# Performance work log

Hardware: AMD Instinct MI355X
Metric: run time of the kernel (lower is better)

Reference implementation:

```python
import jax, jax.numpy as jnp
import numpy as np

N = 100000   # nodes
E = 640000   # edges
F = 128      # num_features
H = 128      # hidden_channels
EPS = 1e-5   # BatchNorm1d eps
SCALE = 0.05


def setup_inputs() -> dict:
    key = jax.random.key(0)
    ks = jax.random.split(key, 16)
    inp = {
        "x": jax.random.normal(ks[0], (N, F), dtype=jnp.float32),
        "edge_index": jax.random.randint(ks[1], (2, E), 0, N, dtype=jnp.int32),
    }
    dims = [(F, H), (H, H), (H, H)]
    k = 2
    for i, (din, dout) in enumerate(dims):
        inp[f"Wl{i}"] = jax.random.normal(ks[k], (dout, din), dtype=jnp.float32) * SCALE
        inp[f"bl{i}"] = jax.random.normal(ks[k + 1], (dout,), dtype=jnp.float32) * SCALE
        inp[f"Wr{i}"] = jax.random.normal(ks[k + 2], (dout, din), dtype=jnp.float32) * SCALE
        k += 3
    inp["W1"] = jax.random.normal(ks[k], (H, H), dtype=jnp.float32) * SCALE
    inp["b1"] = jax.random.normal(ks[k + 1], (H,), dtype=jnp.float32) * SCALE
    inp["W2"] = jax.random.normal(ks[k + 2], (2, H), dtype=jnp.float32) * SCALE
    inp["b2"] = jax.random.normal(ks[k + 3], (2,), dtype=jnp.float32) * SCALE
    return inp


def _batchnorm(x):
    # BatchNorm1d(track_running_stats=False, affine=False): biased batch stats
    mu = jnp.mean(x, axis=0)
    var = jnp.var(x, axis=0)
    return (x - mu) / jnp.sqrt(var + EPS)


def _sage_conv(x, src, dst, Wl, bl, Wr):
    # PyG SAGEConv (aggr='mean'): out = lin_l(mean_agg(x[src] -> dst)) + lin_r(x)
    msg = x[src]                                             # [E, din]
    ssum = jax.ops.segment_sum(msg, dst, num_segments=N)     # [N, din]
    cnt = jax.ops.segment_sum(jnp.ones((E,), x.dtype), dst, num_segments=N)
    agg = ssum / jnp.maximum(cnt, 1.0)[:, None]              # mean, 0 for isolated
    return agg @ Wl.T + bl + x @ Wr.T


def reference(x, edge_index, Wl0, bl0, Wr0, Wl1, bl1, Wr1, Wl2, bl2, Wr2, W1, b1, W2, b2):
    src, dst = edge_index[0], edge_index[1]
    for Wl, bl, Wr in ((Wl0, bl0, Wr0), (Wl1, bl1, Wr1), (Wl2, bl2, Wr2)):
        x = jax.nn.relu(_batchnorm(_sage_conv(x, src, dst, Wl, bl, Wr)))
    x = jax.nn.relu(_batchnorm(x @ W1.T + b1))
    return x @ W2.T + b2
```

## Files before the change

kernel.cpp:

```cpp
#include <hip/hip_runtime.h>
#include <stdint.h>

typedef __bf16 v8bf __attribute__((ext_vector_type(8)));
typedef float f32x4 __attribute__((ext_vector_type(4)));
typedef float f32x2 __attribute__((ext_vector_type(2)));

__device__ __forceinline__ float b2f(unsigned short u) {
    unsigned int x = ((unsigned int)u) << 16;
    return __builtin_bit_cast(float, x);
}
__device__ __forceinline__ float b2f_lo(unsigned int v) {
    return __builtin_bit_cast(float, v << 16);
}
__device__ __forceinline__ float b2f_hi(unsigned int v) {
    return __builtin_bit_cast(float, v & 0xffff0000u);
}
__device__ __forceinline__ unsigned short f2b(float f) {
    unsigned int x = __builtin_bit_cast(unsigned int, f);
    unsigned int r = (x + 0x7fffu + ((x >> 16) & 1u)) >> 16;
    return (unsigned short)r;
}

__device__ __forceinline__ void load_lds16(const void* g, void* l) {
    __builtin_amdgcn_global_load_lds(
        (__attribute__((address_space(1))) void*)(const void*)g,
        (__attribute__((address_space(3))) void*)l, 16, 0, 0);
}

__device__ __forceinline__ void barrier_raw() {
    __builtin_amdgcn_sched_barrier(0);
    __builtin_amdgcn_s_barrier();
    __builtin_amdgcn_sched_barrier(0);
}

#define VMW(n) asm volatile("s_waitcnt vmcnt(" #n ")" ::: "memory")

struct WSrc { const float* p[7]; const float* s[6]; };

__global__ void k_prologue(WSrc w, unsigned short* __restrict__ wbuf,
                           const int* __restrict__ src, const int* __restrict__ dst,
                           int* __restrict__ pos, int* __restrict__ csr, int E,
                           const float* __restrict__ x, unsigned short* __restrict__ xcat,
                           unsigned short* __restrict__ y,
                           int n, int nFill, int nCvtw, int nCopyx) {
    int bid = blockIdx.x;
    int t = threadIdx.x;
    if (bid < nFill) {
        int i = bid * 256 + t;
        if (i < E) {
            int d = dst[i];
            int p = atomicAdd(&pos[d], 1);
            if (p < 64) csr[((size_t)d << 6) + p] = src[i];
        }
    } else if (bid < nFill + nCvtw) {
        int idx = (bid - nFill) * 256 + t;
        if (idx < 115458) {
            float v;
            if (idx < 114688) {
                v = w.p[idx >> 14][idx & 16383];
            } else {
                int rem = idx - 114688;
                int tt, j;
                if (rem < 512)      { tt = rem >> 7; j = rem & 127; }
                else if (rem < 768) { tt = 4; j = rem - 512; }
                else                { tt = 5; j = rem - 768; }
                v = w.s[tt][j];
            }
            wbuf[idx] = f2b(v);
        } else if (idx < 115458 + 64) {
            int k = idx - 115458;
            if (k < 32) {
                ushort4 z; z.x = z.y = z.z = z.w = 0;
                *(ushort4*)&xcat[(size_t)n * 256 + 128 + k * 4] = z;
            } else {
                ushort4 m; m.x = m.y = m.z = m.w = 0xFF7Fu;
                *(ushort4*)&y[(size_t)n * 128 + (k - 32) * 4] = m;
            }
        }
    } else {
        int T = nCopyx * 256;
        int tid = (bid - nFill - nCvtw) * 256 + t;
        int total = n * 32;
        for (int i0 = tid; i0 < total; i0 += 4 * T) {
#pragma unroll
            for (int u = 0; u < 4; u++) {
                int i = i0 + u * T;
                if (i < total) {
                    int row = i >> 5, c4 = (i & 31) * 4;
                    float4 v = *(const float4*)&x[(size_t)row * 128 + c4];
                    ushort4 o;
                    o.x = f2b(v.x); o.y = f2b(v.y); o.z = f2b(v.z); o.w = f2b(v.w);
                    *(ushort4*)&xcat[(size_t)row * 256 + 128 + c4] = o;
                }
            }
        }
    }
}

__global__ void k_hist(const int* __restrict__ pos, int* __restrict__ hist, int n) {
    __shared__ int lh[32];
    int t = threadIdx.x;
    int i = blockIdx.x * 256 + t;
    if (t < 32) lh[t] = 0;
    __syncthreads();
    if (i < n) atomicAdd(&lh[31 - min(pos[i], 31)], 1);
    __syncthreads();
    if (t < 32) atomicAdd(&hist[t], lh[t]);
}

__global__ void k_order(const int* __restrict__ cnt, const int* __restrict__ hist,
                        int* __restrict__ binpos, int* __restrict__ order, int n) {
    __shared__ int lh[32], gb[32], hloc[32];
    int t = threadIdx.x;
    if (t < 32) { lh[t] = 0; hloc[t] = hist[t]; }
    __syncthreads();
    int i = blockIdx.x * 256 + t;
    int b = 0, r = 0;
    if (i < n) {
        b = 31 - min(cnt[i], 31);
        r = atomicAdd(&lh[b], 1);
    }
    __syncthreads();
    if (t < 32) {
        int off = 0;
        for (int k = 0; k < t; k++) off += hloc[k];
        gb[t] = off + atomicAdd(&binpos[t], lh[t]);
    }
    __syncthreads();
    if (i < n) order[gb[b] + r] = i;
}

__global__ __launch_bounds__(256) void k_agg(const unsigned short* __restrict__ xcat,
                                             const int* __restrict__ cnt, const int* __restrict__ csr,
                                             const int* __restrict__ order,
                                             unsigned short* __restrict__ outL, int n) {
    int t = threadIdx.x;
    int l = t & 15;
    int gbase = (t & 63) & ~15;
    int oi = blockIdx.x * 16 + (t >> 4);
    if (oi >= n) return;
    int d = order[oi];
    size_t s = (size_t)d << 6;
    int deg = cnt[d];
    f32x2 ax[4] = {};
    for (int base = 0; base < deg; base += 16) {
        int myidx = (base + l < deg) ? csr[s + base + l] : n;
        int lim = min(16, deg - base);
        for (int b = 0; b < lim; b += 8) {
            int idx[8];
            uint4 v[8];
#pragma unroll
            for (int u = 0; u < 8; u++) idx[u] = __shfl(myidx, gbase + b + u, 64);
#pragma unroll
            for (int u = 0; u < 8; u++)
                v[u] = *(const uint4*)(xcat + (((unsigned)idx[u]) << 8) + 128u + (unsigned)(l << 3));
#pragma unroll
            for (int u = 0; u < 8; u++) {
                unsigned int uu[4] = {v[u].x, v[u].y, v[u].z, v[u].w};
#pragma unroll
                for (int k = 0; k < 4; k++) {
                    f32x2 tv;
                    tv.x = b2f_lo(uu[k]);
                    tv.y = b2f_hi(uu[k]);
                    ax[k] += tv;
                }
            }
        }
    }
    float ic = 1.0f / (float)max(deg, 1);
    uint4 o;
    unsigned int* op = (unsigned int*)&o;
#pragma unroll
    for (int k = 0; k < 4; k++)
        op[k] = ((unsigned int)f2b(ax[k].y * ic) << 16) | f2b(ax[k].x * ic);
    *(uint4*)&outL[(size_t)d * 256 + l * 8] = o;
}

__global__ __launch_bounds__(256) void k_aggbn(const unsigned short* __restrict__ Y,
                                               const float* __restrict__ statp,
                                               const int* __restrict__ cnt, const int* __restrict__ csr,
                                               const int* __restrict__ order,
                                               unsigned short* __restrict__ xcat, int n, float invN) {
    __shared__ float smu[128], sinv[128], sq[128];
    int t = threadIdx.x;
    if (t < 128) {
        float s = 0.f;
#pragma unroll
        for (int sl = 0; sl < 32; sl++) s += statp[sl * 256 + t];
        smu[t] = s * invN;
    } else {
        int u = t - 128;
        float q = 0.f;
#pragma unroll
        for (int sl = 0; sl < 32; sl++) q += statp[sl * 256 + 128 + u];
        sq[u] = q;
    }
    __syncthreads();
    if (t < 128) {
        float mu = smu[t];
        sinv[t] = rsqrtf(sq[t] * invN - mu * mu + 1e-5f);
    }
    __syncthreads();
    int l = t & 15;
    int gbase = (t & 63) & ~15;
    int oi = blockIdx.x * 16 + (t >> 4);
    if (oi >= n) return;
    int d = order[oi];
    f32x2 mu2[4];
    float iv[8];
#pragma unroll
    for (int k = 0; k < 4; k++) {
        mu2[k].x = smu[l * 8 + 2 * k];
        mu2[k].y = smu[l * 8 + 2 * k + 1];
    }
#pragma unroll
    for (int k = 0; k < 8; k++) iv[k] = sinv[l * 8 + k];
    {
        uint4 vo = *(const uint4*)&Y[(size_t)oi * 128 + l * 8];
        unsigned int uu[4] = {vo.x, vo.y, vo.z, vo.w};
        uint4 o;
        unsigned int* op = (unsigned int*)&o;
#pragma unroll
        for (int k = 0; k < 4; k++) {
            float a = fmaxf((b2f_lo(uu[k]) - mu2[k].x) * iv[2 * k], 0.f);
            float b = fmaxf((b2f_hi(uu[k]) - mu2[k].y) * iv[2 * k + 1], 0.f);
            op[k] = ((unsigned int)f2b(b) << 16) | f2b(a);
        }
        *(uint4*)&xcat[(size_t)oi * 256 + 128 + l * 8] = o;
    }
    size_t s = (size_t)d << 6;
    int deg = cnt[d];
    f32x2 z2 = {0.f, 0.f};
    f32x2 ax[4] = {};
    for (int base = 0; base < deg; base += 16) {
        int myidx = (base + l < deg) ? csr[s + base + l] : n;
        int lim = min(16, deg - base);
        for (int b = 0; b < lim; b += 8) {
            int idx[8];
            uint4 v[8];
#pragma unroll
            for (int u = 0; u < 8; u++) idx[u] = __shfl(myidx, gbase + b + u, 64);
#pragma unroll
            for (int u = 0; u < 8; u++)
                v[u] = *(const uint4*)(Y + (((unsigned)idx[u]) << 7) + (unsigned)(l << 3));
#pragma unroll
            for (int u = 0; u < 8; u++) {
                unsigned int uu[4] = {v[u].x, v[u].y, v[u].z, v[u].w};
#pragma unroll
                for (int k = 0; k < 4; k++) {
                    f32x2 tv;
                    tv.x = b2f_lo(uu[k]);
                    tv.y = b2f_hi(uu[k]);
                    tv = tv - mu2[k];
                    tv = __builtin_elementwise_max(tv, z2);
                    ax[k] += tv;
                }
            }
        }
    }
    float ic = 1.0f / (float)max(deg, 1);
    uint4 o;
    unsigned int* op = (unsigned int*)&o;
#pragma unroll
    for (int k = 0; k < 4; k++)
        op[k] = ((unsigned int)f2b(ax[k].y * (iv[2 * k + 1] * ic)) << 16)
              | f2b(ax[k].x * (iv[2 * k] * ic));
    *(uint4*)&xcat[(size_t)d * 256 + l * 8] = o;
}

#define MFMA4(HB, BUF)                                                              \
    do {                                                                            \
        _Pragma("unroll")                                                           \
        for (int c = 0; c < 4; c++) {                                               \
            v8bf af0 = *(const v8bf*)&As[BUF][c][(l16) * 32 + quad * 8];            \
            v8bf af1 = *(const v8bf*)&As[BUF][c][(16 + l16) * 32 + quad * 8];       \
            acc[0][0] = __builtin_amdgcn_mfma_f32_16x16x32_bf16(wreg[(HB) + c][0], af0, acc[0][0], 0, 0, 0); \
            acc[0][1] = __builtin_amdgcn_mfma_f32_16x16x32_bf16(wreg[(HB) + c][1], af0, acc[0][1], 0, 0, 0); \
            acc[1][0] = __builtin_amdgcn_mfma_f32_16x16x32_bf16(wreg[(HB) + c][0], af1, acc[1][0], 0, 0, 0); \
            acc[1][1] = __builtin_amdgcn_mfma_f32_16x16x32_bf16(wreg[(HB) + c][1], af1, acc[1][1], 0, 0, 0); \
        }                                                                           \
    } while (0)

__global__ __launch_bounds__(256, 3) void k_wgemm(const unsigned short* __restrict__ A, int lda, int aoff,
                                                  const unsigned short* __restrict__ W0,
                                                  const unsigned short* __restrict__ W1,
                                                  const unsigned short* __restrict__ bias,
                                                  unsigned short* __restrict__ Y,
                                                  float* __restrict__ statp, int nrows) {
    __shared__ __align__(16) unsigned short As[2][4][1024];
    int t = threadIdx.x;
    int wv = t >> 6, lane = t & 63;
    int quad = lane >> 4, l16 = lane & 15;

    v8bf wreg[8][2];
#pragma unroll
    for (int c = 0; c < 8; c++) {
        const unsigned short* Wp = (c < 4) ? W0 : W1;
#pragma unroll
        for (int j = 0; j < 2; j++)
            wreg[c][j] = *(const v8bf*)(Wp + (size_t)(wv * 32 + j * 16 + l16) * 128 + (c & 3) * 32 + quad * 8);
    }

    float bn[2][4];
#pragma unroll
    for (int j = 0; j < 2; j++) {
        int c0 = wv * 32 + j * 16 + quad * 4;
        uint2 bu = *(const uint2*)&bias[c0];
        bn[j][0] = b2f_lo(bu.x); bn[j][1] = b2f_hi(bu.x);
        bn[j][2] = b2f_lo(bu.y); bn[j][3] = b2f_hi(bu.y);
    }

    f32x4 cs_[2] = {}, cq_[2] = {};

    int ntiles = (nrows + 31) >> 5;
    int tt = t & 127;
    int half = t >> 7;
    int ar = tt >> 2, ac = (tt & 3) * 8;

    auto stage = [&](int m0, int hb, int buf) {
#pragma unroll
        for (int p2 = 0; p2 < 2; p2++) {
            int slot = p2 * 2 + half;
            int gr = m0 + ar;
            if (gr >= nrows) gr = nrows - 1;
            load_lds16(A + (size_t)gr * lda + aoff + (hb + slot) * 32 + ac,
                       &As[buf][slot][(size_t)ar * 32 + ac]);
        }
    };

    int mt = blockIdx.x;
    stage(mt * 32, 0, 0);
    stage(mt * 32, 4, 1);
    bool first = true;
    for (; mt < ntiles; mt += (int)gridDim.x) {
        int m0 = mt * 32;
        int nxt = mt + (int)gridDim.x;
        int nm0 = (nxt < ntiles) ? nxt * 32 : m0;

        if (first) { VMW(2); } else { VMW(6); }
        barrier_raw();

        f32x4 acc[2][2] = {};
        MFMA4(0, 0);
        barrier_raw();
        stage(nm0, 0, 0);

        VMW(2);
        barrier_raw();
        MFMA4(4, 1);

#pragma unroll
        for (int i = 0; i < 2; i++)
#pragma unroll
            for (int j = 0; j < 2; j++)
#pragma unroll
                for (int u = 0; u < 4; u++)
                    acc[i][j][u] += bn[j][u];
#pragma unroll
        for (int i = 0; i < 2; i++) {
            int row = m0 + i * 16 + l16;
            int srow = (row < nrows) ? row : (nrows + 1);
#pragma unroll
            for (int j = 0; j < 2; j++) {
                int c0 = wv * 32 + j * 16 + quad * 4;
                uint2 o;
                o.x = ((unsigned int)f2b(acc[i][j][1]) << 16) | f2b(acc[i][j][0]);
                o.y = ((unsigned int)f2b(acc[i][j][3]) << 16) | f2b(acc[i][j][2]);
                *(uint2*)&Y[(size_t)srow * 128 + c0] = o;
            }
        }
#pragma unroll
        for (int i = 0; i < 2; i++) {
            int row = m0 + i * 16 + l16;
            if (row < nrows) {
#pragma unroll
                for (int j = 0; j < 2; j++)
#pragma unroll
                    for (int u = 0; u < 4; u++) {
                        float v = acc[i][j][u];
                        cs_[j][u] += v;
                        cq_[j][u] += v * v;
                    }
            }
        }
        barrier_raw();
        stage(nm0, 4, 1);
        first = false;
    }

    float* sp = statp + (blockIdx.x & 31) * 256;
#pragma unroll
    for (int j = 0; j < 2; j++) {
        for (int m = 1; m < 16; m <<= 1) {
#pragma unroll
            for (int u = 0; u < 4; u++) {
                cs_[j][u] += __shfl_xor(cs_[j][u], m, 64);
                cq_[j][u] += __shfl_xor(cq_[j][u], m, 64);
            }
        }
        if (l16 == 0) {
            int c0 = wv * 32 + j * 16 + quad * 4;
#pragma unroll
            for (int u = 0; u < 4; u++) {
                atomicAdd(&sp[c0 + u], cs_[j][u]);
                atomicAdd(&sp[128 + c0 + u], cq_[j][u]);
            }
        }
    }
}

__global__ __launch_bounds__(256) void k_wgemm_bn(const unsigned short* __restrict__ A,
                                                  const float* __restrict__ statp,
                                                  const unsigned short* __restrict__ W0,
                                                  const unsigned short* __restrict__ bias,
                                                  unsigned short* __restrict__ Y,
                                                  float* __restrict__ statp_out,
                                                  int nrows, float invN) {
    __shared__ __align__(16) unsigned short Ws[4][4096];
    __shared__ __align__(16) unsigned short As[4][1024];
    __shared__ float smu[128], sinv[128], sq[128];
    int t = threadIdx.x;
    int wv = t >> 6, lane = t & 63;
    int quad = lane >> 4, l16 = lane & 15;

    for (int c = 0; c < 4; c++) {
        int wkc = c * 32;
#pragma unroll
        for (int q = 0; q < 2; q++) {
            int r = q * 64 + (t >> 2);
            load_lds16(W0 + (size_t)r * 128 + wkc + (t & 3) * 8,
                       &Ws[c][(size_t)r * 32 + (t & 3) * 8]);
        }
    }

    if (t < 128) {
        float s = 0.f;
#pragma unroll
        for (int sl = 0; sl < 32; sl++) s += statp[sl * 256 + t];
        smu[t] = s * invN;
    } else {
        int u = t - 128;
        float q = 0.f;
#pragma unroll
        for (int sl = 0; sl < 32; sl++) q += statp[sl * 256 + 128 + u];
        sq[u] = q;
    }
    __syncthreads();
    if (t < 128) {
        float mu = smu[t];
        sinv[t] = rsqrtf(sq[t] * invN - mu * mu + 1e-5f);
    }
    __syncthreads();

    int c16 = (t & 15) * 8;
    int sch = (t & 15) >> 2;
    int sac = (t & 3) * 8;
    int sr = t >> 4;
    float mu8[8], iv8[8];
#pragma unroll
    for (int k = 0; k < 8; k++) { mu8[k] = smu[c16 + k]; iv8[k] = sinv[c16 + k]; }

    float bn[2][4];
#pragma unroll
    for (int j = 0; j < 2; j++) {
        int c0 = wv * 32 + j * 16 + quad * 4;
        uint2 bu = *(const uint2*)&bias[c0];
        bn[j][0] = b2f_lo(bu.x); bn[j][1] = b2f_hi(bu.x);
        bn[j][2] = b2f_lo(bu.y); bn[j][3] = b2f_hi(bu.y);
    }

    f32x4 cs_[2] = {}, cq_[2] = {};

    int ntiles = (nrows + 31) >> 5;
    int mt = blockIdx.x;
    uint4 ra0, ra1;
    {
        int g0 = min(mt * 32 + sr, nrows - 1);
        int g1 = min(mt * 32 + 16 + sr, nrows - 1);
        ra0 = *(const uint4*)(A + (size_t)g0 * 128 + c16);
        ra1 = *(const uint4*)(A + (size_t)g1 * 128 + c16);
    }
    auto xf = [&](uint4 v) -> uint4 {
        unsigned int uu[4] = {v.x, v.y, v.z, v.w};
        uint4 o; unsigned int* op = (unsigned int*)&o;
#pragma unroll
        for (int k = 0; k < 4; k++) {
            float a = fmaxf((b2f_lo(uu[k]) - mu8[2 * k]) * iv8[2 * k], 0.f);
            float b = fmaxf((b2f_hi(uu[k]) - mu8[2 * k + 1]) * iv8[2 * k + 1], 0.f);
            op[k] = ((unsigned int)f2b(b) << 16) | f2b(a);
        }
        return o;
    };

    for (; mt < ntiles; mt += (int)gridDim.x) {
        int m0 = mt * 32;
        int nxt = mt + (int)gridDim.x;

        VMW(0);
        barrier_raw();
        *(uint4*)&As[sch][(size_t)sr * 32 + sac] = xf(ra0);
        *(uint4*)&As[sch][(size_t)(16 + sr) * 32 + sac] = xf(ra1);
        __syncthreads();

        if (nxt < ntiles) {
            int g0 = min(nxt * 32 + sr, nrows - 1);
            int g1 = min(nxt * 32 + 16 + sr, nrows - 1);
            ra0 = *(const uint4*)(A + (size_t)g0 * 128 + c16);
            ra1 = *(const uint4*)(A + (size_t)g1 * 128 + c16);
        }

        f32x4 acc[2][2] = {};
#pragma unroll
        for (int c = 0; c < 4; c++) {
            v8bf af[2], bfv[2];
#pragma unroll
            for (int i = 0; i < 2; i++)
                af[i] = *(const v8bf*)&As[c][(i * 16 + l16) * 32 + quad * 8];
#pragma unroll
            for (int j = 0; j < 2; j++)
                bfv[j] = *(const v8bf*)&Ws[c][(wv * 32 + j * 16 + l16) * 32 + quad * 8];
#pragma unroll
            for (int i = 0; i < 2; i++)
#pragma unroll
                for (int j = 0; j < 2; j++)
                    acc[i][j] = __builtin_amdgcn_mfma_f32_16x16x32_bf16(bfv[j], af[i], acc[i][j], 0, 0, 0);
        }

#pragma unroll
        for (int i = 0; i < 2; i++)
#pragma unroll
            for (int j = 0; j < 2; j++)
#pragma unroll
                for (int u = 0; u < 4; u++)
                    acc[i][j][u] += bn[j][u];
#pragma unroll
        for (int i = 0; i < 2; i++) {
            int row = m0 + i * 16 + l16;
            int srow = (row < nrows) ? row : (nrows + 1);
#pragma unroll
            for (int j = 0; j < 2; j++) {
                int c0 = wv * 32 + j * 16 + quad * 4;
                uint2 o;
                o.x = ((unsigned int)f2b(acc[i][j][1]) << 16) | f2b(acc[i][j][0]);
                o.y = ((unsigned int)f2b(acc[i][j][3]) << 16) | f2b(acc[i][j][2]);
                *(uint2*)&Y[(size_t)srow * 128 + c0] = o;
            }
        }
#pragma unroll
        for (int i = 0; i < 2; i++) {
            int row = m0 + i * 16 + l16;
            if (row < nrows) {
#pragma unroll
                for (int j = 0; j < 2; j++)
#pragma unroll
                    for (int u = 0; u < 4; u++) {
                        float v = acc[i][j][u];
                        cs_[j][u] += v;
                        cq_[j][u] += v * v;
                    }
            }
        }
    }

    float* sp = statp_out + (blockIdx.x & 31) * 256;
#pragma unroll
    for (int j = 0; j < 2; j++) {
        for (int m = 1; m < 16; m <<= 1) {
#pragma unroll
            for (int u = 0; u < 4; u++) {
                cs_[j][u] += __shfl_xor(cs_[j][u], m, 64);
                cq_[j][u] += __shfl_xor(cq_[j][u], m, 64);
            }
        }
        if (l16 == 0) {
            int c0 = wv * 32 + j * 16 + quad * 4;
#pragma unroll
            for (int u = 0; u < 4; u++) {
                atomicAdd(&sp[c0 + u], cs_[j][u]);
                atomicAdd(&sp[128 + c0 + u], cq_[j][u]);
            }
        }
    }
}

__global__ __launch_bounds__(256) void k_bnfinal(const unsigned short* __restrict__ Y,
                                                 const float* __restrict__ statp,
                                                 const unsigned short* __restrict__ W2,
                                                 const unsigned short* __restrict__ b2v,
                                                 float* __restrict__ out, int n, float invN) {
    __shared__ float smu[128], sinv[128], sq[128];
    int t = threadIdx.x;
    if (t < 128) {
        float s = 0.f;
#pragma unroll
        for (int sl = 0; sl < 32; sl++) s += statp[sl * 256 + t];
        smu[t] = s * invN;
    } else {
        int u = t - 128;
        float q = 0.f;
#pragma unroll
        for (int sl = 0; sl < 32; sl++) q += statp[sl * 256 + 128 + u];
        sq[u] = q;
    }
    __syncthreads();
    if (t < 128) {
        float mu = smu[t];
        sinv[t] = rsqrtf(sq[t] * invN - mu * mu + 1e-5f);
    }
    __syncthreads();
    int l = t & 15;
    int r = blockIdx.x * 16 + (t >> 4);
    if (r >= n) return;
    int f8 = l * 8;
    uint4 v = *(const uint4*)&Y[(size_t)r * 128 + f8];
    uint4 w0v = *(const uint4*)&W2[f8];
    uint4 w1v = *(const uint4*)&W2[128 + f8];
    unsigned int uu[4] = {v.x, v.y, v.z, v.w};
    unsigned int u0[4] = {w0v.x, w0v.y, w0v.z, w0v.w};
    unsigned int u1[4] = {w1v.x, w1v.y, w1v.z, w1v.w};
    float d0 = 0.f, d1 = 0.f;
#pragma unroll
    for (int k = 0; k < 4; k++) {
        int f = f8 + 2 * k;
        float a = fmaxf((b2f_lo(uu[k]) - smu[f]) * sinv[f], 0.f);
        float b = fmaxf((b2f_hi(uu[k]) - smu[f + 1]) * sinv[f + 1], 0.f);
        d0 += a * b2f_lo(u0[k]) + b * b2f_hi(u0[k]);
        d1 += a * b2f_lo(u1[k]) + b * b2f_hi(u1[k]);
    }
    for (int o = 1; o < 16; o <<= 1) {
        d0 += __shfl_xor(d0, o, 64);
        d1 += __shfl_xor(d1, o, 64);
    }
    if (l == 0) {
        float2 o2;
        o2.x = d0 + b2f(b2v[0]);
        o2.y = d1 + b2f(b2v[1]);
        *(float2*)&out[(size_t)r * 2] = o2;
    }
}

extern "C" void kernel_launch(void* const* d_in, const int* in_sizes, int n_in,
                              void* d_out, int out_size, void* d_ws, size_t ws_size,
                              hipStream_t stream) {
    const int N = in_sizes[0] / 128;
    const int E = in_sizes[1] / 2;

    const float* x = (const float*)d_in[0];
    const int* ei = (const int*)d_in[1];
    const int* srcp = ei;
    const int* dstp = ei + E;
    float* out = (float*)d_out;

    char* w = (char*)d_ws;
    auto align256 = [](size_t v) { return (v + 255) & ~(size_t)255; };
    size_t o_xcat = 0;
    size_t o_y    = align256(o_xcat + (size_t)(N + 1) * 256 * 2);
    size_t o_csr  = align256(o_y + (size_t)(N + 2) * 128 * 2);
    size_t o_ord  = align256(o_csr + (size_t)N * 64 * 4);
    size_t o_wbuf = align256(o_ord + (size_t)N * 4);
    size_t o_pos  = align256(o_wbuf + 115712 * 2);
    size_t o_stat = o_pos + (size_t)N * 4;
    size_t o_hist = o_stat + 4 * 8192 * 4;
    size_t o_binp = o_hist + 32 * 4;

    unsigned short* xcat = (unsigned short*)(w + o_xcat);
    unsigned short* y    = (unsigned short*)(w + o_y);
    int* csr = (int*)(w + o_csr);
    int* ord  = (int*)(w + o_ord);
    unsigned short* wbuf = (unsigned short*)(w + o_wbuf);
    int* pos = (int*)(w + o_pos);
    float* stat = (float*)(w + o_stat);
    int* hist = (int*)(w + o_hist);
    int* binp = (int*)(w + o_binp);

    const unsigned short* Wl[3] = {wbuf + 0,      wbuf + 32768, wbuf + 65536};
    const unsigned short* Wr[3] = {wbuf + 16384,  wbuf + 49152, wbuf + 81920};
    const unsigned short* W1b   = wbuf + 98304;
    const unsigned short* bl[3] = {wbuf + 114688, wbuf + 114816, wbuf + 114944};
    const unsigned short* b1b   = wbuf + 115072;
    const unsigned short* W2b   = wbuf + 115200;
    const unsigned short* b2b   = wbuf + 115456;

    WSrc wsrc;
    wsrc.p[0] = (const float*)d_in[2];
    wsrc.p[1] = (const float*)d_in[4];
    wsrc.p[2] = (const float*)d_in[5];
    wsrc.p[3] = (const float*)d_in[7];
    wsrc.p[4] = (const float*)d_in[8];
    wsrc.p[5] = (const float*)d_in[10];
    wsrc.p[6] = (const float*)d_in[11];
    wsrc.s[0] = (const float*)d_in[3];
    wsrc.s[1] = (const float*)d_in[6];
    wsrc.s[2] = (const float*)d_in[9];
    wsrc.s[3] = (const float*)d_in[12];
    wsrc.s[4] = (const float*)d_in[13];
    wsrc.s[5] = (const float*)d_in[14];

    const int NB = (N + 255) / 256;
    const int nFill = (E + 255) / 256;
    const int nCvtw = (115458 + 64 + 255) / 256;
    const int nCopyx = 1024;

    hipMemsetAsync(w + o_pos, 0, (size_t)N * 4 + 4 * 8192 * 4 + 64 * 4, stream);

    k_prologue<<<nFill + nCvtw + nCopyx, 256, 0, stream>>>(wsrc, wbuf, srcp, dstp, pos, csr, E,
                                                           x, xcat, y, N, nFill, nCvtw, nCopyx);
    k_hist<<<NB, 256, 0, stream>>>(pos, hist, N);
    k_order<<<NB, 256, 0, stream>>>(pos, hist, binp, ord, N);

    const int wg_grid = 768;
    const int agg16_grid = (N + 15) / 16;
    const int row16_grid = (N + 15) / 16;
    const float invN = 1.0f / (float)N;

    k_agg<<<agg16_grid, 256, 0, stream>>>(xcat, pos, csr, ord, xcat, N);
    k_wgemm<<<wg_grid, 256, 0, stream>>>(xcat, 256, 0, Wl[0], Wr[0], bl[0], y, stat + 0 * 8192, N);
    for (int i = 1; i < 3; i++) {
        k_aggbn<<<agg16_grid, 256, 0, stream>>>(y, stat + (i - 1) * 8192, pos, csr, ord, xcat, N, invN);
        k_wgemm<<<wg_grid, 256, 0, stream>>>(xcat, 256, 0, Wl[i], Wr[i], bl[i], y, stat + i * 8192, N);
    }
    k_wgemm_bn<<<512, 256, 0, stream>>>(y, stat + 2 * 8192, W1b, b1b, y, stat + 3 * 8192, N, invN);
    k_bnfinal<<<row16_grid, 256, 0, stream>>>(y, stat + 3 * 8192, W2b, b2b, out, N, invN);
}
```

Before: 353.6 us.

## Fuse neighbor aggregation and BN-apply into the SAGE GEMM kernel

```diff
diff --git a/kernel.cpp b/kernel.cpp
--- a/kernel.cpp
+++ b/kernel.cpp
@@ -27,12 +27,6 @@
         (__attribute__((address_space(3))) void*)l, 16, 0, 0);
 }
 
-__device__ __forceinline__ void barrier_raw() {
-    __builtin_amdgcn_sched_barrier(0);
-    __builtin_amdgcn_s_barrier();
-    __builtin_amdgcn_sched_barrier(0);
-}
-
 #define VMW(n) asm volatile("s_waitcnt vmcnt(" #n ")" ::: "memory")
 
 struct WSrc { const float* p[7]; const float* s[6]; };
@@ -41,7 +35,7 @@
                            const int* __restrict__ src, const int* __restrict__ dst,
                            int* __restrict__ pos, int* __restrict__ csr, int E,
                            const float* __restrict__ x, unsigned short* __restrict__ xcat,
-                           unsigned short* __restrict__ y,
+                           unsigned short* __restrict__ ya, unsigned short* __restrict__ yb,
                            int n, int nFill, int nCvtw, int nCopyx) {
     int bid = blockIdx.x;
     int t = threadIdx.x;
@@ -67,14 +61,17 @@
                 v = w.s[tt][j];
             }
             wbuf[idx] = f2b(v);
-        } else if (idx < 115458 + 64) {
+        } else if (idx < 115458 + 96) {
             int k = idx - 115458;
             if (k < 32) {
                 ushort4 z; z.x = z.y = z.z = z.w = 0;
                 *(ushort4*)&xcat[(size_t)n * 256 + 128 + k * 4] = z;
+            } else if (k < 64) {
+                ushort4 m; m.x = m.y = m.z = m.w = 0xFF7Fu;
+                *(ushort4*)&ya[(size_t)n * 128 + (k - 32) * 4] = m;
             } else {
                 ushort4 m; m.x = m.y = m.z = m.w = 0xFF7Fu;
-                *(ushort4*)&y[(size_t)n * 128 + (k - 32) * 4] = m;
+                *(ushort4*)&yb[(size_t)n * 128 + (k - 64) * 4] = m;
             }
         }
     } else {
@@ -97,200 +94,45 @@
     }
 }
 
-__global__ void k_hist(const int* __restrict__ pos, int* __restrict__ hist, int n) {
-    __shared__ int lh[32];
-    int t = threadIdx.x;
-    int i = blockIdx.x * 256 + t;
-    if (t < 32) lh[t] = 0;
-    __syncthreads();
-    if (i < n) atomicAdd(&lh[31 - min(pos[i], 31)], 1);
-    __syncthreads();
-    if (t < 32) atomicAdd(&hist[t], lh[t]);
-}
-
-__global__ void k_order(const int* __restrict__ cnt, const int* __restrict__ hist,
-                        int* __restrict__ binpos, int* __restrict__ order, int n) {
-    __shared__ int lh[32], gb[32], hloc[32];
-    int t = threadIdx.x;
-    if (t < 32) { lh[t] = 0; hloc[t] = hist[t]; }
-    __syncthreads();
-    int i = blockIdx.x * 256 + t;
-    int b = 0, r = 0;
-    if (i < n) {
-        b = 31 - min(cnt[i], 31);
-        r = atomicAdd(&lh[b], 1);
-    }
-    __syncthreads();
-    if (t < 32) {
-        int off = 0;
-        for (int k = 0; k < t; k++) off += hloc[k];
-        gb[t] = off + atomicAdd(&binpos[t], lh[t]);
-    }
-    __syncthreads();
-    if (i < n) order[gb[b] + r] = i;
-}
-
-__global__ __launch_bounds__(256) void k_agg(const unsigned short* __restrict__ xcat,
-                                             const int* __restrict__ cnt, const int* __restrict__ csr,
-                                             const int* __restrict__ order,
-                                             unsigned short* __restrict__ outL, int n) {
-    int t = threadIdx.x;
-    int l = t & 15;
-    int gbase = (t & 63) & ~15;
-    int oi = blockIdx.x * 16 + (t >> 4);
-    if (oi >= n) return;
-    int d = order[oi];
-    size_t s = (size_t)d << 6;
-    int deg = cnt[d];
-    f32x2 ax[4] = {};
-    for (int base = 0; base < deg; base += 16) {
-        int myidx = (base + l < deg) ? csr[s + base + l] : n;
-        int lim = min(16, deg - base);
-        for (int b = 0; b < lim; b += 8) {
-            int idx[8];
-            uint4 v[8];
-#pragma unroll
-            for (int u = 0; u < 8; u++) idx[u] = __shfl(myidx, gbase + b + u, 64);
-#pragma unroll
-            for (int u = 0; u < 8; u++)
-                v[u] = *(const uint4*)(xcat + (((unsigned)idx[u]) << 8) + 128u + (unsigned)(l << 3));
-#pragma unroll
-            for (int u = 0; u < 8; u++) {
-                unsigned int uu[4] = {v[u].x, v[u].y, v[u].z, v[u].w};
-#pragma unroll
-                for (int k = 0; k < 4; k++) {
-                    f32x2 tv;
-                    tv.x = b2f_lo(uu[k]);
-                    tv.y = b2f_hi(uu[k]);
-                    ax[k] += tv;
-                }
-            }
-        }
-    }
-    float ic = 1.0f / (float)max(deg, 1);
-    uint4 o;
-    unsigned int* op = (unsigned int*)&o;
-#pragma unroll
-    for (int k = 0; k < 4; k++)
-        op[k] = ((unsigned int)f2b(ax[k].y * ic) << 16) | f2b(ax[k].x * ic);
-    *(uint4*)&outL[(size_t)d * 256 + l * 8] = o;
-}
-
-__global__ __launch_bounds__(256) void k_aggbn(const unsigned short* __restrict__ Y,
-                                               const float* __restrict__ statp,
-                                               const int* __restrict__ cnt, const int* __restrict__ csr,
-                                               const int* __restrict__ order,
-                                               unsigned short* __restrict__ xcat, int n, float invN) {
-    __shared__ float smu[128], sinv[128], sq[128];
-    int t = threadIdx.x;
-    if (t < 128) {
-        float s = 0.f;
-#pragma unroll
-        for (int sl = 0; sl < 32; sl++) s += statp[sl * 256 + t];
-        smu[t] = s * invN;
-    } else {
-        int u = t - 128;
-        float q = 0.f;
-#pragma unroll
-        for (int sl = 0; sl < 32; sl++) q += statp[sl * 256 + 128 + u];
-        sq[u] = q;
-    }
-    __syncthreads();
-    if (t < 128) {
-        float mu = smu[t];
-        sinv[t] = rsqrtf(sq[t] * invN - mu * mu + 1e-5f);
-    }
-    __syncthreads();
-    int l = t & 15;
-    int gbase = (t & 63) & ~15;
-    int oi = blockIdx.x * 16 + (t >> 4);
-    if (oi >= n) return;
-    int d = order[oi];
-    f32x2 mu2[4];
-    float iv[8];
-#pragma unroll
-    for (int k = 0; k < 4; k++) {
-        mu2[k].x = smu[l * 8 + 2 * k];
-        mu2[k].y = smu[l * 8 + 2 * k + 1];
-    }
-#pragma unroll
-    for (int k = 0; k < 8; k++) iv[k] = sinv[l * 8 + k];
-    {
-        uint4 vo = *(const uint4*)&Y[(size_t)oi * 128 + l * 8];
-        unsigned int uu[4] = {vo.x, vo.y, vo.z, vo.w};
-        uint4 o;
-        unsigned int* op = (unsigned int*)&o;
-#pragma unroll
-        for (int k = 0; k < 4; k++) {
-            float a = fmaxf((b2f_lo(uu[k]) - mu2[k].x) * iv[2 * k], 0.f);
-            float b = fmaxf((b2f_hi(uu[k]) - mu2[k].y) * iv[2 * k + 1], 0.f);
-            op[k] = ((unsigned int)f2b(b) << 16) | f2b(a);
-        }
-        *(uint4*)&xcat[(size_t)oi * 256 + 128 + l * 8] = o;
-    }
-    size_t s = (size_t)d << 6;
-    int deg = cnt[d];
-    f32x2 z2 = {0.f, 0.f};
-    f32x2 ax[4] = {};
-    for (int base = 0; base < deg; base += 16) {
-        int myidx = (base + l < deg) ? csr[s + base + l] : n;
-        int lim = min(16, deg - base);
-        for (int b = 0; b < lim; b += 8) {
-            int idx[8];
-            uint4 v[8];
-#pragma unroll
-            for (int u = 0; u < 8; u++) idx[u] = __shfl(myidx, gbase + b + u, 64);
-#pragma unroll
-            for (int u = 0; u < 8; u++)
-                v[u] = *(const uint4*)(Y + (((unsigned)idx[u]) << 7) + (unsigned)(l << 3));
-#pragma unroll
-            for (int u = 0; u < 8; u++) {
-                unsigned int uu[4] = {v[u].x, v[u].y, v[u].z, v[u].w};
-#pragma unroll
-                for (int k = 0; k < 4; k++) {
-                    f32x2 tv;
-                    tv.x = b2f_lo(uu[k]);
-                    tv.y = b2f_hi(uu[k]);
-                    tv = tv - mu2[k];
-                    tv = __builtin_elementwise_max(tv, z2);
-                    ax[k] += tv;
-                }
-            }
-        }
-    }
-    float ic = 1.0f / (float)max(deg, 1);
-    uint4 o;
-    unsigned int* op = (unsigned int*)&o;
-#pragma unroll
-    for (int k = 0; k < 4; k++)
-        op[k] = ((unsigned int)f2b(ax[k].y * (iv[2 * k + 1] * ic)) << 16)
-              | f2b(ax[k].x * (iv[2 * k] * ic));
-    *(uint4*)&xcat[(size_t)d * 256 + l * 8] = o;
-}
-
-#define MFMA4(HB, BUF)                                                              \
-    do {                                                                            \
-        _Pragma("unroll")                                                           \
-        for (int c = 0; c < 4; c++) {                                               \
-            v8bf af0 = *(const v8bf*)&As[BUF][c][(l16) * 32 + quad * 8];            \
-            v8bf af1 = *(const v8bf*)&As[BUF][c][(16 + l16) * 32 + quad * 8];       \
-            acc[0][0] = __builtin_amdgcn_mfma_f32_16x16x32_bf16(wreg[(HB) + c][0], af0, acc[0][0], 0, 0, 0); \
-            acc[0][1] = __builtin_amdgcn_mfma_f32_16x16x32_bf16(wreg[(HB) + c][1], af0, acc[0][1], 0, 0, 0); \
-            acc[1][0] = __builtin_amdgcn_mfma_f32_16x16x32_bf16(wreg[(HB) + c][0], af1, acc[1][0], 0, 0, 0); \
-            acc[1][1] = __builtin_amdgcn_mfma_f32_16x16x32_bf16(wreg[(HB) + c][1], af1, acc[1][1], 0, 0, 0); \
-        }                                                                           \
-    } while (0)
-
-__global__ __launch_bounds__(256, 3) void k_wgemm(const unsigned short* __restrict__ A, int lda, int aoff,
+template<bool BN>
+__global__ __launch_bounds__(256, 3) void k_fused(const unsigned short* __restrict__ S, int slda, int soff,
+                                                  const float* __restrict__ statp,
+                                                  const int* __restrict__ cnt, const int* __restrict__ csr,
                                                   const unsigned short* __restrict__ W0,
                                                   const unsigned short* __restrict__ W1,
                                                   const unsigned short* __restrict__ bias,
                                                   unsigned short* __restrict__ Y,
-                                                  float* __restrict__ statp, int nrows) {
-    __shared__ __align__(16) unsigned short As[2][4][1024];
+                                                  float* __restrict__ statp_out,
+                                                  int n, float invN) {
+    __shared__ __align__(16) unsigned short As[8][1024];
+    __shared__ float smu[128], sinv[128], sq[128];
     int t = threadIdx.x;
     int wv = t >> 6, lane = t & 63;
     int quad = lane >> 4, l16 = lane & 15;
+    int grp = t >> 4;
+    int l = t & 15;
+    int gbase = (t & 63) & ~15;
+
+    if constexpr (BN) {
+        if (t < 128) {
+            float s = 0.f;
+#pragma unroll
+            for (int sl = 0; sl < 32; sl++) s += statp[sl * 256 + t];
+            smu[t] = s * invN;
+        } else {
+            int u = t - 128;
+            float q = 0.f;
+#pragma unroll
+            for (int sl = 0; sl < 32; sl++) q += statp[sl * 256 + 128 + u];
+            sq[u] = q;
+        }
+        __syncthreads();
+        if (t < 128) {
+            float mu = smu[t];
+            sinv[t] = rsqrtf(sq[t] * invN - mu * mu + 1e-5f);
+        }
+        __syncthreads();
+    }
 
     v8bf wreg[8][2];
 #pragma unroll
@@ -300,7 +142,6 @@
         for (int j = 0; j < 2; j++)
             wreg[c][j] = *(const v8bf*)(Wp + (size_t)(wv * 32 + j * 16 + l16) * 128 + (c & 3) * 32 + quad * 8);
     }
-
     float bn[2][4];
 #pragma unroll
     for (int j = 0; j < 2; j++) {
@@ -310,45 +151,102 @@
         bn[j][2] = b2f_lo(bu.y); bn[j][3] = b2f_hi(bu.y);
     }
 
+    f32x2 mu2[4];
+    float iv8[8];
+    if constexpr (BN) {
+#pragma unroll
+        for (int k = 0; k < 4; k++) {
+            mu2[k].x = smu[l * 8 + 2 * k];
+            mu2[k].y = smu[l * 8 + 2 * k + 1];
+        }
+#pragma unroll
+        for (int k = 0; k < 8; k++) iv8[k] = sinv[l * 8 + k];
+    }
+
     f32x4 cs_[2] = {}, cq_[2] = {};
-
-    int ntiles = (nrows + 31) >> 5;
-    int tt = t & 127;
-    int half = t >> 7;
-    int ar = tt >> 2, ac = (tt & 3) * 8;
-
-    auto stage = [&](int m0, int hb, int buf) {
-#pragma unroll
-        for (int p2 = 0; p2 < 2; p2++) {
-            int slot = p2 * 2 + half;
-            int gr = m0 + ar;
-            if (gr >= nrows) gr = nrows - 1;
-            load_lds16(A + (size_t)gr * lda + aoff + (hb + slot) * 32 + ac,
-                       &As[buf][slot][(size_t)ar * 32 + ac]);
-        }
-    };
-
-    int mt = blockIdx.x;
-    stage(mt * 32, 0, 0);
-    stage(mt * 32, 4, 1);
-    bool first = true;
-    for (; mt < ntiles; mt += (int)gridDim.x) {
+    int ntiles = (n + 31) >> 5;
+
+    for (int mt = blockIdx.x; mt < ntiles; mt += (int)gridDim.x) {
         int m0 = mt * 32;
-        int nxt = mt + (int)gridDim.x;
-        int nm0 = (nxt < ntiles) ? nxt * 32 : m0;
-
-        if (first) { VMW(2); } else { VMW(6); }
-        barrier_raw();
+#pragma unroll
+        for (int p = 0; p < 2; p++) {
+            int r = p * 16 + grp;
+            int d = m0 + r;
+            int dd = (d < n) ? d : (n - 1);
+            uint4 vo = *(const uint4*)(S + (size_t)dd * slda + soff + l * 8);
+            uint4 ow;
+            if constexpr (BN) {
+                unsigned int uu[4] = {vo.x, vo.y, vo.z, vo.w};
+                unsigned int* op = (unsigned int*)&ow;
+#pragma unroll
+                for (int k = 0; k < 4; k++) {
+                    float a = fmaxf((b2f_lo(uu[k]) - mu2[k].x) * iv8[2 * k], 0.f);
+                    float b = fmaxf((b2f_hi(uu[k]) - mu2[k].y) * iv8[2 * k + 1], 0.f);
+                    op[k] = ((unsigned int)f2b(b) << 16) | f2b(a);
+                }
+            } else {
+                ow = vo;
+            }
+            *(uint4*)&As[4 + (l >> 2)][r * 32 + (l & 3) * 8] = ow;
+            int deg = (d < n) ? cnt[dd] : 0;
+            size_t s = (size_t)dd << 6;
+            f32x2 z2 = {0.f, 0.f};
+            f32x2 ax[4] = {};
+            for (int base = 0; base < deg; base += 16) {
+                int myidx = (base + l < deg) ? csr[s + base + l] : n;
+                int lim = min(16, deg - base);
+                for (int b = 0; b < lim; b += 8) {
+                    int idx[8];
+                    uint4 v[8];
+#pragma unroll
+                    for (int u = 0; u < 8; u++) idx[u] = __shfl(myidx, gbase + b + u, 64);
+#pragma unroll
+                    for (int u = 0; u < 8; u++)
+                        v[u] = *(const uint4*)(S + (size_t)(unsigned)idx[u] * slda + soff + (unsigned)(l << 3));
+#pragma unroll
+                    for (int u = 0; u < 8; u++) {
+                        unsigned int uu[4] = {v[u].x, v[u].y, v[u].z, v[u].w};
+#pragma unroll
+                        for (int k = 0; k < 4; k++) {
+                            f32x2 tv;
+                            tv.x = b2f_lo(uu[k]);
+                            tv.y = b2f_hi(uu[k]);
+                            if constexpr (BN) {
+                                tv = tv - mu2[k];
+                                tv = __builtin_elementwise_max(tv, z2);
+                            }
+                            ax[k] += tv;
+                        }
+                    }
+                }
+            }
+            float ic = 1.0f / (float)max(deg, 1);
+            uint4 ag;
+            unsigned int* ap = (unsigned int*)&ag;
+            if constexpr (BN) {
+#pragma unroll
+                for (int k = 0; k < 4; k++)
+                    ap[k] = ((unsigned int)f2b(ax[k].y * (iv8[2 * k + 1] * ic)) << 16)
+                          | f2b(ax[k].x * (iv8[2 * k] * ic));
+            } else {
+#pragma unroll
+                for (int k = 0; k < 4; k++)
+                    ap[k] = ((unsigned int)f2b(ax[k].y * ic) << 16) | f2b(ax[k].x * ic);
+            }
+            *(uint4*)&As[l >> 2][r * 32 + (l & 3) * 8] = ag;
+        }
+        __syncthreads();
 
         f32x4 acc[2][2] = {};
-        MFMA4(0, 0);
-        barrier_raw();
-        stage(nm0, 0, 0);
-
-        VMW(2);
-        barrier_raw();
-        MFMA4(4, 1);
-
+#pragma unroll
+        for (int c = 0; c < 8; c++) {
+            v8bf af0 = *(const v8bf*)&As[c][(l16) * 32 + quad * 8];
+            v8bf af1 = *(const v8bf*)&As[c][(16 + l16) * 32 + quad * 8];
+            acc[0][0] = __builtin_amdgcn_mfma_f32_16x16x32_bf16(wreg[c][0], af0, acc[0][0], 0, 0, 0);
+            acc[0][1] = __builtin_amdgcn_mfma_f32_16x16x32_bf16(wreg[c][1], af0, acc[0][1], 0, 0, 0);
+            acc[1][0] = __builtin_amdgcn_mfma_f32_16x16x32_bf16(wreg[c][0], af1, acc[1][0], 0, 0, 0);
+            acc[1][1] = __builtin_amdgcn_mfma_f32_16x16x32_bf16(wreg[c][1], af1, acc[1][1], 0, 0, 0);
+        }
 #pragma unroll
         for (int i = 0; i < 2; i++)
 #pragma unroll
@@ -359,7 +257,7 @@
 #pragma unroll
         for (int i = 0; i < 2; i++) {
             int row = m0 + i * 16 + l16;
-            int srow = (row < nrows) ? row : (nrows + 1);
+            int srow = (row < n) ? row : (n + 1);
 #pragma unroll
             for (int j = 0; j < 2; j++) {
                 int c0 = wv * 32 + j * 16 + quad * 4;
@@ -372,7 +270,7 @@
 #pragma unroll
         for (int i = 0; i < 2; i++) {
             int row = m0 + i * 16 + l16;
-            if (row < nrows) {
+            if (row < n) {
 #pragma unroll
                 for (int j = 0; j < 2; j++)
 #pragma unroll
@@ -383,12 +281,10 @@
                     }
             }
         }
-        barrier_raw();
-        stage(nm0, 4, 1);
-        first = false;
-    }
-
-    float* sp = statp + (blockIdx.x & 31) * 256;
+        __syncthreads();
+    }
+
+    float* sp = statp_out + (blockIdx.x & 31) * 256;
 #pragma unroll
     for (int j = 0; j < 2; j++) {
         for (int m = 1; m < 16; m <<= 1) {
@@ -497,7 +393,9 @@
         int nxt = mt + (int)gridDim.x;
 
         VMW(0);
-        barrier_raw();
+        __builtin_amdgcn_sched_barrier(0);
+        __builtin_amdgcn_s_barrier();
+        __builtin_amdgcn_sched_barrier(0);
         *(uint4*)&As[sch][(size_t)sr * 32 + sac] = xf(ra0);
         *(uint4*)&As[sch][(size_t)(16 + sr) * 32 + sac] = xf(ra1);
         __syncthreads();
@@ -654,24 +552,20 @@
     char* w = (char*)d_ws;
     auto align256 = [](size_t v) { return (v + 255) & ~(size_t)255; };
     size_t o_xcat = 0;
-    size_t o_y    = align256(o_xcat + (size_t)(N + 1) * 256 * 2);
-    size_t o_csr  = align256(o_y + (size_t)(N + 2) * 128 * 2);
-    size_t o_ord  = align256(o_csr + (size_t)N * 64 * 4);
-    size_t o_wbuf = align256(o_ord + (size_t)N * 4);
+    size_t o_ya   = align256(o_xcat + (size_t)(N + 1) * 256 * 2);
+    size_t o_yb   = align256(o_ya + (size_t)(N + 2) * 128 * 2);
+    size_t o_csr  = align256(o_yb + (size_t)(N + 2) * 128 * 2);
+    size_t o_wbuf = align256(o_csr + (size_t)N * 64 * 4);
     size_t o_pos  = align256(o_wbuf + 115712 * 2);
     size_t o_stat = o_pos + (size_t)N * 4;
-    size_t o_hist = o_stat + 4 * 8192 * 4;
-    size_t o_binp = o_hist + 32 * 4;
 
     unsigned short* xcat = (unsigned short*)(w + o_xcat);
-    unsigned short* y    = (unsigned short*)(w + o_y);
+    unsigned short* ya   = (unsigned short*)(w + o_ya);
+    unsigned short* yb   = (unsigned short*)(w + o_yb);
     int* csr = (int*)(w + o_csr);
-    int* ord  = (int*)(w + o_ord);
     unsigned short* wbuf = (unsigned short*)(w + o_wbuf);
     int* pos = (int*)(w + o_pos);
     float* stat = (float*)(w + o_stat);
-    int* hist = (int*)(w + o_hist);
-    int* binp = (int*)(w + o_binp);
 
     const unsigned short* Wl[3] = {wbuf + 0,      wbuf + 32768, wbuf + 65536};
     const unsigned short* Wr[3] = {wbuf + 16384,  wbuf + 49152, wbuf + 81920};
@@ -696,29 +590,25 @@
     wsrc.s[4] = (const float*)d_in[13];
     wsrc.s[5] = (const float*)d_in[14];
 
-    const int NB = (N + 255) / 256;
     const int nFill = (E + 255) / 256;
-    const int nCvtw = (115458 + 64 + 255) / 256;
+    const int nCvtw = (115458 + 96 + 255) / 256;
     const int nCopyx = 1024;
 
-    hipMemsetAsync(w + o_pos, 0, (size_t)N * 4 + 4 * 8192 * 4 + 64 * 4, stream);
+    hipMemsetAsync(w + o_pos, 0, (size_t)N * 4 + 4 * 8192 * 4, stream);
 
     k_prologue<<<nFill + nCvtw + nCopyx, 256, 0, stream>>>(wsrc, wbuf, srcp, dstp, pos, csr, E,
-                                                           x, xcat, y, N, nFill, nCvtw, nCopyx);
-    k_hist<<<NB, 256, 0, stream>>>(pos, hist, N);
-    k_order<<<NB, 256, 0, stream>>>(pos, hist, binp, ord, N);
-
-    const int wg_grid = 768;
-    const int agg16_grid = (N + 15) / 16;
+                                                           x, xcat, ya, yb, N, nFill, nCvtw, nCopyx);
+
+    const int fgrid = 768;
     const int row16_grid = (N + 15) / 16;
     const float invN = 1.0f / (float)N;
 
-    k_agg<<<agg16_grid, 256, 0, stream>>>(xcat, pos, csr, ord, xcat, N);
-    k_wgemm<<<wg_grid, 256, 0, stream>>>(xcat, 256, 0, Wl[0], Wr[0], bl[0], y, stat + 0 * 8192, N);
-    for (int i = 1; i < 3; i++) {
-        k_aggbn<<<agg16_grid, 256, 0, stream>>>(y, stat + (i - 1) * 8192, pos, csr, ord, xcat, N, invN);
-        k_wgemm<<<wg_grid, 256, 0, stream>>>(xcat, 256, 0, Wl[i], Wr[i], bl[i], y, stat + i * 8192, N);
-    }
-    k_wgemm_bn<<<512, 256, 0, stream>>>(y, stat + 2 * 8192, W1b, b1b, y, stat + 3 * 8192, N, invN);
-    k_bnfinal<<<row16_grid, 256, 0, stream>>>(y, stat + 3 * 8192, W2b, b2b, out, N, invN);
-}
+    k_fused<false><<<fgrid, 256, 0, stream>>>(xcat, 256, 128, nullptr, pos, csr,
+                                              Wl[0], Wr[0], bl[0], ya, stat + 0 * 8192, N, invN);
+    k_fused<true><<<fgrid, 256, 0, stream>>>(ya, 128, 0, stat + 0 * 8192, pos, csr,
+                                             Wl[1], Wr[1], bl[1], yb, stat + 1 * 8192, N, invN);
+    k_fused<true><<<fgrid, 256, 0, stream>>>(yb, 128, 0, stat + 1 * 8192, pos, csr,
+                                             Wl[2], Wr[2], bl[2], ya, stat + 2 * 8192, N, invN);
+    k_wgemm_bn<<<512, 256, 0, stream>>>(ya, stat + 2 * 8192, W1b, b1b, ya, stat + 3 * 8192, N, invN);
+    k_bnfinal<<<row16_grid, 256, 0, stream>>>(ya, stat + 3 * 8192, W2b, b2b, out, N, invN);
+}
```

Measured after the change: 328.5 us (median of 2 runs). 7.1% less time.
